# Kernel tuning notes

Hardware: AMD Instinct MI355X
Metric: run time of the kernel (lower is better)

Reference implementation:

```python
import jax, jax.numpy as jnp
import numpy as np

NUM_HEADS = 12
HEAD_SIZE = 64
HIDDEN = NUM_HEADS * HEAD_SIZE  # 768
SEQ = 4096


def setup_inputs() -> dict:
    key = jax.random.key(0)
    ks = jax.random.split(key, 7)
    s = 0.02
    return {
        "hidden_states": jax.random.normal(ks[0], (1, SEQ, HIDDEN), jnp.float32),
        "attention_mask": jnp.zeros((1, 1, 1, SEQ), jnp.float32),
        "Wq": jax.random.normal(ks[1], (HIDDEN, HIDDEN), jnp.float32) * s,
        "bq": jax.random.normal(ks[2], (HIDDEN,), jnp.float32) * s,
        "Wk": jax.random.normal(ks[3], (HIDDEN, HIDDEN), jnp.float32) * s,
        "bk": jax.random.normal(ks[4], (HIDDEN,), jnp.float32) * s,
        "Wv": jax.random.normal(ks[5], (HIDDEN, HIDDEN), jnp.float32) * s,
        "bv": jax.random.normal(ks[6], (HIDDEN,), jnp.float32) * s,
    }


def _split_heads(x):
    # [B, S, H] -> [B, nh, S, hd]
    B, S, _ = x.shape
    return x.reshape(B, S, NUM_HEADS, HEAD_SIZE).transpose(0, 2, 1, 3)


def reference(hidden_states, attention_mask, Wq, bq, Wk, bk, Wv, bv):
    # torch Linear: y = x @ W.T + b
    q = _split_heads(hidden_states @ Wq.T + bq)  # [B, nh, S, hd]
    k = _split_heads(hidden_states @ Wk.T + bk)
    scores = jnp.einsum("bhqd,bhkd->bhqk", q, k) / jnp.sqrt(
        jnp.asarray(HEAD_SIZE, hidden_states.dtype)
    )
    scores = scores + attention_mask  # broadcast [1,1,1,S]
    probs = jax.nn.softmax(scores, axis=-1)  # [B, nh, S, S]
    # multi_rand_attn_cuda is a Monte-Carlo approximation of the exact
    # aggregation: probs @ (hidden @ Wv.T + bv), per head. The reference
    # computes the exact expected value (deterministic equivalent).
    v = _split_heads(hidden_states @ Wv.T + bv)  # [B, nh, S, hd]
    ctx = jnp.einsum("bhqk,bhkd->bhqd", probs, v)  # [B, nh, S, hd]
    B, _, S, _ = ctx.shape
    ctx = ctx.transpose(0, 2, 1, 3).reshape(B, S, HIDDEN)
    return ctx
```

## Files before the change

kernel.cpp:

```cpp
#include <hip/hip_runtime.h>
#include <hip/hip_bf16.h>

#define SEQ 4096
#define HID 768
#define NHEAD 12
#define HDIM 64
#define KVB 64
#define NT (SEQ / KVB)
#define PBK 64
#define PNT (HID / PBK)

typedef __attribute__((ext_vector_type(8))) short bf16x8;
typedef __attribute__((ext_vector_type(4))) float f32x4;
typedef __attribute__((ext_vector_type(4))) short s16x4;

static __device__ __forceinline__ short f2bf(float f) {
    unsigned u = __builtin_bit_cast(unsigned, f);
    unsigned r = (u + 0x7fffu + ((u >> 16) & 1u)) >> 16;
    return (short)r;
}
static __device__ __forceinline__ float bf2f(unsigned short u) {
    return __builtin_bit_cast(float, (unsigned)u << 16);
}
static __device__ __forceinline__ unsigned cvtpk(float lo, float hi) {
    unsigned r;
    asm("v_cvt_pk_bf16_f32 %0, %1, %2" : "=v"(r) : "v"(lo), "v"(hi));
    return r;
}
static __device__ __forceinline__ float max3f(float a, float b, float c) {
    float r;
    asm("v_max3_f32 %0, %1, %2, %3" : "=v"(r) : "v"(a), "v"(b), "v"(c));
    return r;
}
static __device__ __forceinline__ void glds16(const void* g, void* l) {
    __builtin_amdgcn_global_load_lds(
        (const __attribute__((address_space(1))) unsigned*)g,
        (__attribute__((address_space(3))) unsigned*)l, 16, 0, 0);
}

__global__ __launch_bounds__(256) void cast_bf16_kernel(
    const float* __restrict__ src, short* __restrict__ dst)
{
    const size_t i = (size_t)blockIdx.x * 256 + threadIdx.x;
    const float4* s = reinterpret_cast<const float4*>(src) + i * 2;
    const float4 a = s[0], b = s[1];
    bf16x8 o;
    o[0] = f2bf(a.x); o[1] = f2bf(a.y); o[2] = f2bf(a.z); o[3] = f2bf(a.w);
    o[4] = f2bf(b.x); o[5] = f2bf(b.y); o[6] = f2bf(b.z); o[7] = f2bf(b.w);
    reinterpret_cast<bf16x8*>(dst)[i] = o;
}

__global__ __launch_bounds__(256) void cast_w_kernel(
    const float* __restrict__ Wq, const float* __restrict__ Wk,
    const float* __restrict__ Wv, short* __restrict__ dst)
{
    const int z = blockIdx.y;
    const float* src = (z == 0) ? Wq : ((z == 1) ? Wk : Wv);
    const size_t i = (size_t)blockIdx.x * 256 + threadIdx.x;
    const float4* s = reinterpret_cast<const float4*>(src) + i * 2;
    const float4 a = s[0], b = s[1];
    bf16x8 o;
    o[0] = f2bf(a.x); o[1] = f2bf(a.y); o[2] = f2bf(a.z); o[3] = f2bf(a.w);
    o[4] = f2bf(b.x); o[5] = f2bf(b.y); o[6] = f2bf(b.z); o[7] = f2bf(b.w);
    reinterpret_cast<bf16x8*>(dst + (size_t)z * HID * HID)[i] = o;
}

__global__ __launch_bounds__(256) void qkv_proj_kernel(
    const short* __restrict__ hsb, const short* __restrict__ Wb,
    const float* __restrict__ bq, const float* __restrict__ bk,
    const float* __restrict__ bv,
    short* __restrict__ Qb, short* __restrict__ Kb, short* __restrict__ Vt)
{
    __shared__ __align__(16) char lds[65536];
    const int z = blockIdx.z;
    const float* bias = (z == 0) ? bq : ((z == 1) ? bk : bv);

    const int lane = threadIdx.x & 63;
    const int w    = threadIdx.x >> 6;
    const int lr = lane & 15, hi = lane >> 4;
    const int wi = w >> 1, wj = w & 1;

    const short* Ag; const short* Bg; int ar0, br0;
    if (z < 2) { Ag = Wb + (size_t)z * HID * HID; ar0 = blockIdx.x * 128;
                 Bg = hsb;                        br0 = blockIdx.y * 128; }
    else       { Ag = hsb;                        ar0 = blockIdx.y * 128;
                 Bg = Wb + (size_t)2 * HID * HID; br0 = blockIdx.x * 128; }

    const int rsub = lane >> 3;
    const int c16  = (lane & 7) ^ rsub;

    auto stage = [&](int t, int buf) {
        const int k0 = t * PBK;
#pragma unroll
        for (int c = 0; c < 4; ++c) {
            const int ch = w * 4 + c;
            const int row = ch * 8 + rsub;
            glds16(Ag + (size_t)(ar0 + row) * HID + k0 + c16 * 8,
                   lds + buf * 16384 + ch * 1024);
            glds16(Bg + (size_t)(br0 + row) * HID + k0 + c16 * 8,
                   lds + 32768 + buf * 16384 + ch * 1024);
        }
    };

    stage(0, 0);
    f32x4 acc[4][4] = {};

    for (int t = 0; t < PNT; ++t) {
        asm volatile("s_waitcnt vmcnt(0)" ::: "memory");
        __builtin_amdgcn_s_barrier();
        __builtin_amdgcn_sched_barrier(0);
        if (t + 1 < PNT) stage(t + 1, (t + 1) & 1);
        const char* LA = lds + (t & 1) * 16384;
        const char* LB = lds + 32768 + (t & 1) * 16384;
#pragma unroll
        for (int ks = 0; ks < 2; ++ks) {
            bf16x8 af[4], bf_[4];
#pragma unroll
            for (int i = 0; i < 4; ++i) {
                const int rowA = wi * 64 + i * 16 + lr;
                af[i] = *reinterpret_cast<const bf16x8*>(
                    LA + rowA * 128 + (((ks * 4 + hi) ^ (rowA & 7)) << 4));
                const int rowB = wj * 64 + i * 16 + lr;
                bf_[i] = *reinterpret_cast<const bf16x8*>(
                    LB + rowB * 128 + (((ks * 4 + hi) ^ (rowB & 7)) << 4));
            }
            __builtin_amdgcn_s_setprio(1);
#pragma unroll
            for (int ia = 0; ia < 4; ++ia)
#pragma unroll
                for (int ib = 0; ib < 4; ++ib)
                    acc[ia][ib] = __builtin_amdgcn_mfma_f32_16x16x32_bf16(
                        af[ia], bf_[ib], acc[ia][ib], 0, 0, 0);
            __builtin_amdgcn_s_setprio(0);
        }
    }

    const float SCQ = 0.125f * 1.44269504088896340736f;
    if (z < 2) {
        short* outp = (z == 0) ? Qb : Kb;
        const float sc = (z == 0) ? SCQ : 1.0f;
#pragma unroll
        for (int ia = 0; ia < 4; ++ia) {
            const int nb = ar0 + wi * 64 + ia * 16 + hi * 4;
            const float4 b4 = *reinterpret_cast<const float4*>(bias + nb);
#pragma unroll
            for (int ib = 0; ib < 4; ++ib) {
                const int m = br0 + wj * 64 + ib * 16 + lr;
                s16x4 v;
                v[0] = f2bf((acc[ia][ib][0] + b4.x) * sc);
                v[1] = f2bf((acc[ia][ib][1] + b4.y) * sc);
                v[2] = f2bf((acc[ia][ib][2] + b4.z) * sc);
                v[3] = f2bf((acc[ia][ib][3] + b4.w) * sc);
                *reinterpret_cast<s16x4*>(outp + (size_t)m * HID + nb) = v;
            }
        }
    } else {
#pragma unroll
        for (int ib = 0; ib < 4; ++ib) {
            const int n = br0 + wj * 64 + ib * 16 + lr;
            const float bb = bias[n];
#pragma unroll
            for (int ia = 0; ia < 4; ++ia) {
                const int mb = ar0 + wi * 64 + ia * 16 + hi * 4;
                s16x4 v;
                v[0] = f2bf(acc[ia][ib][0] + bb);
                v[1] = f2bf(acc[ia][ib][1] + bb);
                v[2] = f2bf(acc[ia][ib][2] + bb);
                v[3] = f2bf(acc[ia][ib][3] + bb);
                *reinterpret_cast<s16x4*>(Vt + (size_t)n * SEQ + mb) = v;
            }
        }
    }
}

__global__ __launch_bounds__(256, 4) void attn_kernel(
    const short* __restrict__ Qb, const short* __restrict__ Kb,
    const short* __restrict__ Vt, const float* __restrict__ maskp,
    float* __restrict__ out)
{
    __shared__ __align__(16) char lds[40960];
    const int tid  = threadIdx.x;
    const int lane = tid & 63;
    const int w    = tid >> 6;
    const int lr = lane & 15, hi = lane >> 4;
    const int qh = w >> 1, kh = w & 1;
    const int h  = blockIdx.y;
    const int q0 = blockIdx.x * 32 + qh * 16;
    const float ML = 1.44269504088896340736f;

    const int srow = lane >> 3;
    auto stage = [&](int t, int buf) {
        const int kt = t * KVB;
#pragma unroll
        for (int j = 0; j < 2; ++j) {
            const int ch  = w * 2 + j;
            const int row = ch * 8 + srow;
            const int c16 = (lane & 7) ^ srow ^ ((ch & 1) << 2);
            glds16(Kb + (size_t)(kt + row) * HID + h * HDIM + c16 * 8,
                   lds + buf * 8192 + ch * 1024);
            glds16(Vt + (size_t)(h * HDIM + row) * SEQ + kt + c16 * 8,
                   lds + 16384 + buf * 8192 + ch * 1024);
        }
    };

    stage(0, 0);

    {
        short* mb = (short*)(lds + 32768);
        const int base = tid * 16;
        float4 m4[4];
#pragma unroll
        for (int i = 0; i < 4; ++i)
            m4[i] = *reinterpret_cast<const float4*>(maskp + base + i * 4);
        union { unsigned u[8]; } pk;
#pragma unroll
        for (int i = 0; i < 4; ++i) {
            pk.u[i * 2]     = cvtpk(m4[i].x * ML, m4[i].y * ML);
            pk.u[i * 2 + 1] = cvtpk(m4[i].z * ML, m4[i].w * ML);
        }
        *reinterpret_cast<uint4*>(mb + base)     = *reinterpret_cast<uint4*>(&pk.u[0]);
        *reinterpret_cast<uint4*>(mb + base + 8) = *reinterpret_cast<uint4*>(&pk.u[4]);
    }

    const short* qp = Qb + (size_t)(q0 + lr) * HID + h * HDIM + hi * 8;
    const bf16x8 qf0 = *reinterpret_cast<const bf16x8*>(qp);
    const bf16x8 qf1 = *reinterpret_cast<const bf16x8*>(qp + 32);

    __syncthreads();

    f32x4 acc[4] = {};
    float m_r = -INFINITY, ls = 0.f;
    const int kbase = ((lr >> 2) * 8) + (lr & 3) + kh * 32;
    const int fv    = (lr & 7) ^ (((lr >> 3) & 1) << 2);
    const int vslot = ((kh * 4 + hi) ^ fv) << 4;
    const short* mlds = (const short*)(lds + 32768);

    for (int t = 0; t < NT; ++t) {
        asm volatile("s_waitcnt vmcnt(0)" ::: "memory");
        __builtin_amdgcn_s_barrier();
        __builtin_amdgcn_sched_barrier(0);
        if (t + 1 < NT) stage(t + 1, (t + 1) & 1);

        const bf16x8 mv = *reinterpret_cast<const bf16x8*>(
            mlds + t * KVB + kh * 32 + hi * 8);
        f32x4 ci0, ci1;
#pragma unroll
        for (int r = 0; r < 4; ++r) {
            ci0[r] = bf2f((unsigned short)mv[r]);
            ci1[r] = bf2f((unsigned short)mv[4 + r]);
        }

        const char* KT = lds + (t & 1) * 8192;
        float s2[2][4];
#pragma unroll
        for (int kg = 0; kg < 2; ++kg) {
            const int row = kbase + kg * 4;
            const int fr  = (row & 7) ^ ((row >> 1) & 4);
            const bf16x8 kf0 = *reinterpret_cast<const bf16x8*>(
                KT + row * 128 + ((hi ^ fr) << 4));
            const bf16x8 kf1 = *reinterpret_cast<const bf16x8*>(
                KT + row * 128 + (((4 + hi) ^ fr) << 4));
            f32x4 zz = (kg == 0) ? ci0 : ci1;
            __builtin_amdgcn_s_setprio(1);
            zz = __builtin_amdgcn_mfma_f32_16x16x32_bf16(kf0, qf0, zz, 0, 0, 0);
            zz = __builtin_amdgcn_mfma_f32_16x16x32_bf16(kf1, qf1, zz, 0, 0, 0);
            __builtin_amdgcn_s_setprio(0);
            s2[kg][0] = zz[0]; s2[kg][1] = zz[1];
            s2[kg][2] = zz[2]; s2[kg][3] = zz[3];
        }

        float e_[2][4];
#pragma unroll
        for (int kg = 0; kg < 2; ++kg)
#pragma unroll
            for (int r = 0; r < 4; ++r)
                e_[kg][r] = exp2f(s2[kg][r] - m_r);

        const float pa = max3f(e_[0][0], e_[0][1], e_[0][2]);
        const float pb = max3f(e_[0][3], e_[1][0], e_[1][1]);
        const float pc = max3f(e_[1][2], e_[1][3], pa);
        const float pmax = fmaxf(pb, pc);
        if (__ballot(pmax > 256.f)) {
            float t_ = fmaxf(
                max3f(s2[0][0], s2[0][1], s2[0][2]),
                max3f(fmaxf(s2[0][3], s2[1][0]),
                      fmaxf(s2[1][1], s2[1][2]), s2[1][3]));
            t_ = fmaxf(t_, __shfl_xor(t_, 16));
            t_ = fmaxf(t_, __shfl_xor(t_, 32));
            const float newm = fmaxf(m_r, t_);
            const float sc = exp2f(fmaxf(m_r - newm, -128.f));
            ls *= sc;
#pragma unroll
            for (int dg = 0; dg < 4; ++dg) acc[dg] *= sc;
            m_r = newm;
#pragma unroll
            for (int kg = 0; kg < 2; ++kg)
#pragma unroll
                for (int r = 0; r < 4; ++r)
                    e_[kg][r] = exp2f(s2[kg][r] - newm);
        }

        ls += ((e_[0][0] + e_[0][1]) + (e_[0][2] + e_[0][3]))
            + ((e_[1][0] + e_[1][1]) + (e_[1][2] + e_[1][3]));
        union { unsigned u[4]; bf16x8 v; } P;
        P.u[0] = cvtpk(e_[0][0], e_[0][1]);
        P.u[1] = cvtpk(e_[0][2], e_[0][3]);
        P.u[2] = cvtpk(e_[1][0], e_[1][1]);
        P.u[3] = cvtpk(e_[1][2], e_[1][3]);

        const char* VT = lds + 16384 + (t & 1) * 8192;
#pragma unroll
        for (int dg = 0; dg < 4; ++dg) {
            const bf16x8 vf = *reinterpret_cast<const bf16x8*>(
                VT + (dg * 16 + lr) * 128 + vslot);
            __builtin_amdgcn_s_setprio(1);
            acc[dg] = __builtin_amdgcn_mfma_f32_16x16x32_bf16(vf, P.v, acc[dg], 0, 0, 0);
            __builtin_amdgcn_s_setprio(0);
        }
    }

    {
        float t_ = ls;
        t_ += __shfl_xor(t_, 16);
        t_ += __shfl_xor(t_, 32);
        ls = t_;
    }

    __syncthreads();
    float* mg  = (float*)lds;
    float* mlb = (float*)(lds + 8192);
    if (kh == 1) {
        float2 v0; v0.x = m_r; v0.y = ls;
        *reinterpret_cast<float2*>(mlb + (qh * 64 + lane) * 2) = v0;
#pragma unroll
        for (int dg = 0; dg < 4; ++dg)
            *reinterpret_cast<f32x4*>(
                mg + ((qh * 4 + dg) * 64 + lane) * 4) = acc[dg];
    }
    __syncthreads();
    if (kh == 0) {
        const float2 v = *reinterpret_cast<const float2*>(
            mlb + (qh * 64 + lane) * 2);
        const float mm = fmaxf(m_r, v.x);
        const float sc0 = exp2f(fmaxf(m_r - mm, -128.f));
        const float sc1 = exp2f(fmaxf(v.x - mm, -128.f));
        const float rl = 1.0f / (ls * sc0 + v.y * sc1);
#pragma unroll
        for (int dg = 0; dg < 4; ++dg) {
            const f32x4 o1 = *reinterpret_cast<const f32x4*>(
                mg + ((qh * 4 + dg) * 64 + lane) * 4);
            const f32x4 of = (acc[dg] * sc0 + o1 * sc1) * rl;
            float* op = out + (size_t)(q0 + lr) * HID + h * HDIM + dg * 16 + hi * 4;
            *reinterpret_cast<f32x4*>(op) = of;
        }
    }
}

extern "C" void kernel_launch(void* const* d_in, const int* in_sizes, int n_in,
                              void* d_out, int out_size, void* d_ws, size_t ws_size,
                              hipStream_t stream) {
    const float* hs   = (const float*)d_in[0];
    const float* mask = (const float*)d_in[1];
    const float* Wq   = (const float*)d_in[2];
    const float* bq   = (const float*)d_in[3];
    const float* Wk   = (const float*)d_in[4];
    const float* bk   = (const float*)d_in[5];
    const float* Wv   = (const float*)d_in[6];
    const float* bv   = (const float*)d_in[7];

    short* Qb = (short*)d_ws;
    short* Kb = Qb + (size_t)SEQ * HID;
    short* Vt = Kb + (size_t)SEQ * HID;
    float* out = (float*)d_out;

    short* hsb = (short*)d_out;
    short* Wb  = hsb + (size_t)SEQ * HID;

    cast_bf16_kernel<<<dim3(SEQ * HID / 2048), 256, 0, stream>>>(hs, hsb);
    cast_w_kernel<<<dim3(HID * HID / 2048, 3), 256, 0, stream>>>(Wq, Wk, Wv, Wb);

    qkv_proj_kernel<<<dim3(HID / 128, SEQ / 128, 3), 256, 0, stream>>>(
        hsb, Wb, bq, bk, bv, Qb, Kb, Vt);

    attn_kernel<<<dim3(SEQ / 32, NHEAD), 256, 0, stream>>>(Qb, Kb, Vt, mask, out);
}
```

Measured before the change: 151.9 us.

## Widen attention blocks to 512 threads sharing each K/V tile, store mask as fp32

The attention kernel now runs 8 waves per block and covers 64 query rows instead of 32. Each staged K/V tile in LDS is therefore reused by twice as many queries, and each wave issues one async load per tile instead of two. The mask is kept in LDS as fp32, so the per-tile bf16 unpack goes away. LDS pointers and swizzle offsets are precomputed outside the loop, and the loop is unrolled by two with fixed buffer indices. In exchange the kernel uses more LDS and runs with fewer blocks, and the launch bound of 512 threads with 6 blocks may be unreachable, which could push register pressure up.

After: 132.6 us. 12.7% less time.

```diff
diff --git a/kernel.cpp b/kernel.cpp
--- a/kernel.cpp
+++ b/kernel.cpp
@@ -18,9 +18,6 @@
     unsigned u = __builtin_bit_cast(unsigned, f);
     unsigned r = (u + 0x7fffu + ((u >> 16) & 1u)) >> 16;
     return (short)r;
-}
-static __device__ __forceinline__ float bf2f(unsigned short u) {
-    return __builtin_bit_cast(float, (unsigned)u << 16);
 }
 static __device__ __forceinline__ unsigned cvtpk(float lo, float hi) {
     unsigned r;
@@ -173,118 +170,105 @@
     }
 }
 
-__global__ __launch_bounds__(256, 4) void attn_kernel(
+__global__ __launch_bounds__(512, 6) void attn_kernel(
     const short* __restrict__ Qb, const short* __restrict__ Kb,
     const short* __restrict__ Vt, const float* __restrict__ maskp,
     float* __restrict__ out)
 {
-    __shared__ __align__(16) char lds[40960];
+    __shared__ __align__(16) char lds[49152];
     const int tid  = threadIdx.x;
     const int lane = tid & 63;
     const int w    = tid >> 6;
     const int lr = lane & 15, hi = lane >> 4;
     const int qh = w >> 1, kh = w & 1;
-    const int h  = blockIdx.y;
-    const int q0 = blockIdx.x * 32 + qh * 16;
+    const int head = blockIdx.y;
+    const int q0 = blockIdx.x * 64 + qh * 16;
     const float ML = 1.44269504088896340736f;
 
     const int srow = lane >> 3;
-    auto stage = [&](int t, int buf) {
-        const int kt = t * KVB;
-#pragma unroll
-        for (int j = 0; j < 2; ++j) {
-            const int ch  = w * 2 + j;
-            const int row = ch * 8 + srow;
-            const int c16 = (lane & 7) ^ srow ^ ((ch & 1) << 2);
-            glds16(Kb + (size_t)(kt + row) * HID + h * HDIM + c16 * 8,
-                   lds + buf * 8192 + ch * 1024);
-            glds16(Vt + (size_t)(h * HDIM + row) * SEQ + kt + c16 * 8,
-                   lds + 16384 + buf * 8192 + ch * 1024);
-        }
+    const int c16s = (lane & 7) ^ srow ^ ((w & 1) << 2);
+    const int sofK = (w * 8 + srow) * HID + head * HDIM + c16s * 8;
+    const int sofV = (head * HDIM + w * 8 + srow) * SEQ + c16s * 8;
+    const short* gK = Kb;
+    const short* gV = Vt;
+    char* sdK = lds + w * 1024;
+    char* sdV = lds + 16384 + w * 1024;
+
+    auto stagep = [&](int buf) {
+        glds16(gK + sofK, sdK + buf * 8192);
+        glds16(gV + sofV, sdV + buf * 8192);
+        gK += KVB * HID; gV += KVB;
     };
 
-    stage(0, 0);
+    stagep(0);
 
     {
-        short* mb = (short*)(lds + 32768);
-        const int base = tid * 16;
-        float4 m4[4];
-#pragma unroll
-        for (int i = 0; i < 4; ++i)
-            m4[i] = *reinterpret_cast<const float4*>(maskp + base + i * 4);
-        union { unsigned u[8]; } pk;
-#pragma unroll
-        for (int i = 0; i < 4; ++i) {
-            pk.u[i * 2]     = cvtpk(m4[i].x * ML, m4[i].y * ML);
-            pk.u[i * 2 + 1] = cvtpk(m4[i].z * ML, m4[i].w * ML);
-        }
-        *reinterpret_cast<uint4*>(mb + base)     = *reinterpret_cast<uint4*>(&pk.u[0]);
-        *reinterpret_cast<uint4*>(mb + base + 8) = *reinterpret_cast<uint4*>(&pk.u[4]);
-    }
-
-    const short* qp = Qb + (size_t)(q0 + lr) * HID + h * HDIM + hi * 8;
+        float* mb = (float*)(lds + 32768);
+        const int base = tid * 8;
+#pragma unroll
+        for (int i = 0; i < 2; ++i) {
+            float4 m4 = *reinterpret_cast<const float4*>(maskp + base + i * 4);
+            m4.x *= ML; m4.y *= ML; m4.z *= ML; m4.w *= ML;
+            *reinterpret_cast<float4*>(mb + base + i * 4) = m4;
+        }
+    }
+
+    const short* qp = Qb + (size_t)(q0 + lr) * HID + head * HDIM + hi * 8;
     const bf16x8 qf0 = *reinterpret_cast<const bf16x8*>(qp);
     const bf16x8 qf1 = *reinterpret_cast<const bf16x8*>(qp + 32);
 
     __syncthreads();
 
+    const int kbase = ((lr >> 2) * 8) + (lr & 3);
+    const int krow0 = kh * 32 + kbase;
+    const int fr0   = (krow0 & 7) ^ (((krow0 >> 3) & 1) << 2);
+    const int o1    = (hi ^ fr0) << 4;
+    const char* kpA = lds + krow0 * 128 + o1;
+    const char* kpB = lds + krow0 * 128 + (o1 ^ 64);
+    const int fv    = (lr & 7) ^ (((lr >> 3) & 1) << 2);
+    const char* vpB = lds + 16384 + lr * 128 + (((kh * 4 + hi) ^ fv) << 4);
+    const float* mptr = (const float*)(lds + 32768) + kh * 32 + hi * 8;
+
     f32x4 acc[4] = {};
     float m_r = -INFINITY, ls = 0.f;
-    const int kbase = ((lr >> 2) * 8) + (lr & 3) + kh * 32;
-    const int fv    = (lr & 7) ^ (((lr >> 3) & 1) << 2);
-    const int vslot = ((kh * 4 + hi) ^ fv) << 4;
-    const short* mlds = (const short*)(lds + 32768);
-
-    for (int t = 0; t < NT; ++t) {
+
+    auto tile = [&](int tt, int buf) {
         asm volatile("s_waitcnt vmcnt(0)" ::: "memory");
         __builtin_amdgcn_s_barrier();
         __builtin_amdgcn_sched_barrier(0);
-        if (t + 1 < NT) stage(t + 1, (t + 1) & 1);
-
-        const bf16x8 mv = *reinterpret_cast<const bf16x8*>(
-            mlds + t * KVB + kh * 32 + hi * 8);
-        f32x4 ci0, ci1;
+        if (tt + 1 < NT) stagep(buf ^ 1);
+
+        const f32x4 ci0 = *reinterpret_cast<const f32x4*>(mptr);
+        const f32x4 ci1 = *reinterpret_cast<const f32x4*>(mptr + 4);
+        mptr += KVB;
+        const int bo = buf * 8192;
+        const bf16x8 kf00 = *reinterpret_cast<const bf16x8*>(kpA + bo);
+        const bf16x8 kf01 = *reinterpret_cast<const bf16x8*>(kpB + bo);
+        const bf16x8 kf10 = *reinterpret_cast<const bf16x8*>(kpB + bo + 512);
+        const bf16x8 kf11 = *reinterpret_cast<const bf16x8*>(kpA + bo + 512);
+        f32x4 z0 = ci0, z1 = ci1;
+        __builtin_amdgcn_s_setprio(1);
+        z0 = __builtin_amdgcn_mfma_f32_16x16x32_bf16(kf00, qf0, z0, 0, 0, 0);
+        z0 = __builtin_amdgcn_mfma_f32_16x16x32_bf16(kf01, qf1, z0, 0, 0, 0);
+        z1 = __builtin_amdgcn_mfma_f32_16x16x32_bf16(kf10, qf0, z1, 0, 0, 0);
+        z1 = __builtin_amdgcn_mfma_f32_16x16x32_bf16(kf11, qf1, z1, 0, 0, 0);
+        __builtin_amdgcn_s_setprio(0);
+
+        float e0[4], e1[4];
 #pragma unroll
         for (int r = 0; r < 4; ++r) {
-            ci0[r] = bf2f((unsigned short)mv[r]);
-            ci1[r] = bf2f((unsigned short)mv[4 + r]);
-        }
-
-        const char* KT = lds + (t & 1) * 8192;
-        float s2[2][4];
-#pragma unroll
-        for (int kg = 0; kg < 2; ++kg) {
-            const int row = kbase + kg * 4;
-            const int fr  = (row & 7) ^ ((row >> 1) & 4);
-            const bf16x8 kf0 = *reinterpret_cast<const bf16x8*>(
-                KT + row * 128 + ((hi ^ fr) << 4));
-            const bf16x8 kf1 = *reinterpret_cast<const bf16x8*>(
-                KT + row * 128 + (((4 + hi) ^ fr) << 4));
-            f32x4 zz = (kg == 0) ? ci0 : ci1;
-            __builtin_amdgcn_s_setprio(1);
-            zz = __builtin_amdgcn_mfma_f32_16x16x32_bf16(kf0, qf0, zz, 0, 0, 0);
-            zz = __builtin_amdgcn_mfma_f32_16x16x32_bf16(kf1, qf1, zz, 0, 0, 0);
-            __builtin_amdgcn_s_setprio(0);
-            s2[kg][0] = zz[0]; s2[kg][1] = zz[1];
-            s2[kg][2] = zz[2]; s2[kg][3] = zz[3];
-        }
-
-        float e_[2][4];
-#pragma unroll
-        for (int kg = 0; kg < 2; ++kg)
-#pragma unroll
-            for (int r = 0; r < 4; ++r)
-                e_[kg][r] = exp2f(s2[kg][r] - m_r);
-
-        const float pa = max3f(e_[0][0], e_[0][1], e_[0][2]);
-        const float pb = max3f(e_[0][3], e_[1][0], e_[1][1]);
-        const float pc = max3f(e_[1][2], e_[1][3], pa);
+            e0[r] = exp2f(z0[r] - m_r);
+            e1[r] = exp2f(z1[r] - m_r);
+        }
+
+        const float pa = max3f(e0[0], e0[1], e0[2]);
+        const float pb = max3f(e0[3], e1[0], e1[1]);
+        const float pc = max3f(e1[2], e1[3], pa);
         const float pmax = fmaxf(pb, pc);
         if (__ballot(pmax > 256.f)) {
             float t_ = fmaxf(
-                max3f(s2[0][0], s2[0][1], s2[0][2]),
-                max3f(fmaxf(s2[0][3], s2[1][0]),
-                      fmaxf(s2[1][1], s2[1][2]), s2[1][3]));
+                max3f(z0[0], z0[1], z0[2]),
+                max3f(fmaxf(z0[3], z1[0]), fmaxf(z1[1], z1[2]), z1[3]));
             t_ = fmaxf(t_, __shfl_xor(t_, 16));
             t_ = fmaxf(t_, __shfl_xor(t_, 32));
             const float newm = fmaxf(m_r, t_);
@@ -294,41 +278,42 @@
             for (int dg = 0; dg < 4; ++dg) acc[dg] *= sc;
             m_r = newm;
 #pragma unroll
-            for (int kg = 0; kg < 2; ++kg)
-#pragma unroll
-                for (int r = 0; r < 4; ++r)
-                    e_[kg][r] = exp2f(s2[kg][r] - newm);
-        }
-
-        ls += ((e_[0][0] + e_[0][1]) + (e_[0][2] + e_[0][3]))
-            + ((e_[1][0] + e_[1][1]) + (e_[1][2] + e_[1][3]));
+            for (int r = 0; r < 4; ++r) {
+                e0[r] = exp2f(z0[r] - newm);
+                e1[r] = exp2f(z1[r] - newm);
+            }
+        }
+
+        ls += ((e0[0] + e0[1]) + (e0[2] + e0[3]))
+            + ((e1[0] + e1[1]) + (e1[2] + e1[3]));
         union { unsigned u[4]; bf16x8 v; } P;
-        P.u[0] = cvtpk(e_[0][0], e_[0][1]);
-        P.u[1] = cvtpk(e_[0][2], e_[0][3]);
-        P.u[2] = cvtpk(e_[1][0], e_[1][1]);
-        P.u[3] = cvtpk(e_[1][2], e_[1][3]);
-
-        const char* VT = lds + 16384 + (t & 1) * 8192;
+        P.u[0] = cvtpk(e0[0], e0[1]);
+        P.u[1] = cvtpk(e0[2], e0[3]);
+        P.u[2] = cvtpk(e1[0], e1[1]);
+        P.u[3] = cvtpk(e1[2], e1[3]);
+
+        __builtin_amdgcn_s_setprio(1);
 #pragma unroll
         for (int dg = 0; dg < 4; ++dg) {
             const bf16x8 vf = *reinterpret_cast<const bf16x8*>(
-                VT + (dg * 16 + lr) * 128 + vslot);
-            __builtin_amdgcn_s_setprio(1);
+                vpB + bo + dg * 2048);
             acc[dg] = __builtin_amdgcn_mfma_f32_16x16x32_bf16(vf, P.v, acc[dg], 0, 0, 0);
-            __builtin_amdgcn_s_setprio(0);
-        }
-    }
-
-    {
-        float t_ = ls;
-        t_ += __shfl_xor(t_, 16);
-        t_ += __shfl_xor(t_, 32);
-        ls = t_;
-    }
+        }
+        __builtin_amdgcn_s_setprio(0);
+    };
+
+#pragma unroll 1
+    for (int t = 0; t < NT; t += 2) {
+        tile(t, 0);
+        tile(t + 1, 1);
+    }
+
+    ls += __shfl_xor(ls, 16);
+    ls += __shfl_xor(ls, 32);
 
     __syncthreads();
     float* mg  = (float*)lds;
-    float* mlb = (float*)(lds + 8192);
+    float* mlb = (float*)(lds + 16384);
     if (kh == 1) {
         float2 v0; v0.x = m_r; v0.y = ls;
         *reinterpret_cast<float2*>(mlb + (qh * 64 + lane) * 2) = v0;
@@ -347,10 +332,11 @@
         const float rl = 1.0f / (ls * sc0 + v.y * sc1);
 #pragma unroll
         for (int dg = 0; dg < 4; ++dg) {
-            const f32x4 o1 = *reinterpret_cast<const f32x4*>(
+            const f32x4 o1v = *reinterpret_cast<const f32x4*>(
                 mg + ((qh * 4 + dg) * 64 + lane) * 4);
-            const f32x4 of = (acc[dg] * sc0 + o1 * sc1) * rl;
-            float* op = out + (size_t)(q0 + lr) * HID + h * HDIM + dg * 16 + hi * 4;
+            const f32x4 of = (acc[dg] * sc0 + o1v * sc1) * rl;
+            float* op = out + (size_t)(q0 + lr) * HID
+                      + head * HDIM + dg * 16 + hi * 4;
             *reinterpret_cast<f32x4*>(op) = of;
         }
     }
@@ -382,5 +368,5 @@
     qkv_proj_kernel<<<dim3(HID / 128, SEQ / 128, 3), 256, 0, stream>>>(
         hsb, Wb, bq, bk, bv, Qb, Kb, Vt);
 
-    attn_kernel<<<dim3(SEQ / 32, NHEAD), 256, 0, stream>>>(Qb, Kb, Vt, mask, out);
-}
+    attn_kernel<<<dim3(SEQ / KVB, NHEAD), 512, 0, stream>>>(Qb, Kb, Vt, mask, out);
+}
```
